# Kernel tuning notes

Hardware: AMD Instinct MI355X
Metric: run time of the kernel (lower is better)

## Reference

```python
import jax, jax.numpy as jnp
import numpy as np

BEAM = 64  # min(beam_size=64, num_states=512)


def setup_inputs() -> dict:
    key = jax.random.key(0)
    ks = jax.random.split(key, 8)
    B, N, S, E, F, D = 8, 1024, 512, 2048, 256, 32
    unaries = jax.random.normal(ks[0], (B, N, S), jnp.float32)
    masks = jnp.ones((B, N), dtype=bool)
    binary_edges = jax.random.randint(ks[1], (B, E, 2), 0, N)
    binary_masks = jnp.ones((B, E), dtype=bool)
    node_features = jax.random.normal(ks[2], (B, N, F), jnp.float32)
    targets = jax.random.randint(ks[3], (B, N), 0, S)
    # learned params
    bin_embed = jax.random.uniform(ks[4], (2, S, D), jnp.float32)  # torch.rand init
    W_dyn = jax.random.normal(ks[5], (2 * F, D * D), jnp.float32) / jnp.sqrt(2.0 * F)
    b_dyn = jnp.zeros((D * D,), jnp.float32)
    return dict(unaries=unaries, masks=masks, binary_edges=binary_edges,
                binary_masks=binary_masks, node_features=node_features,
                targets=targets, bin_embed=bin_embed, W_dyn=W_dyn, b_dyn=b_dyn)


def reference(unaries, masks, binary_edges, binary_masks, node_features,
              targets, bin_embed, W_dyn, b_dyn):
    B, N, S = unaries.shape
    D = bin_embed.shape[-1]
    mf = masks.astype(unaries.dtype)
    un = unaries * mf[..., None]  # mask unaries

    # put target state first in the beam (scatter +inf, then topk indices)
    big = jnp.asarray(1e30, un.dtype)
    _un = jax.lax.stop_gradient(un).at[
        jnp.arange(B)[:, None], jnp.arange(N)[None, :], targets].set(big)
    _, beam_targets = jax.lax.top_k(_un, BEAM)               # [B,N,K] int
    beam_unary = jnp.take_along_axis(un, beam_targets, axis=2)  # [B,N,K]

    # gather beam state-ids and node features at edge endpoints
    e0, e1 = binary_edges[..., 0], binary_edges[..., 1]      # [B,E]
    bt0 = jnp.take_along_axis(beam_targets, e0[:, :, None], axis=1)  # [B,E,K]
    bt1 = jnp.take_along_axis(beam_targets, e1[:, :, None], axis=1)
    s0 = bin_embed[0][bt0]                                   # [B,E,K,D]
    s1 = bin_embed[1][bt1]                                   # [B,E,K,D]
    f0 = jnp.take_along_axis(node_features, e0[:, :, None], axis=1)  # [B,E,F]
    f1 = jnp.take_along_axis(node_features, e1[:, :, None], axis=1)
    feat = jnp.concatenate([f0, f1], axis=-1)                # [B,E,2F]
    ew = jax.nn.relu(feat @ W_dyn + b_dyn)                   # [B,E,D*D]
    ew = ew.reshape(B, -1, D, D)                             # [B,E,D,D]

    # low-rank binary potentials: B E K1 D1, B E D1 D2, B E K2 D2 -> B E K1 K2
    bin_phis = jnp.einsum('beki,beij,belj->bekl', s0, ew, s1)

    # piecewise pseudo-likelihood
    norm_unary = jax.nn.log_softmax(beam_unary, axis=-1)
    gold_unary = jnp.where(masks, norm_unary[:, :, 0], 0.0)
    pll = gold_unary.sum(-1)                                 # [B]

    E = bin_phis.shape[1]
    norm_bin = jax.nn.log_softmax(bin_phis.reshape(B, E, BEAM * BEAM), axis=-1)
    gold_bin = jnp.where(binary_masks, norm_bin[:, :, 0], 0.0)  # index (0,0)
    pll = pll + gold_bin.sum(-1)

    nll = -(pll / mf.sum(-1)).mean()
    return nll
```

## Files before the change

### kernel.cpp

```cpp
#include <hip/hip_runtime.h>
#include <hip/hip_bf16.h>
#include <math.h>

#define BATCH  8
#define NNODE  1024
#define NSTATE 512
#define NEDGE  2048
#define NFEAT  256
#define DDIM   32
#define KBEAM  64

typedef __attribute__((ext_vector_type(8))) short bf16x8;
typedef __attribute__((ext_vector_type(4))) float f32x4;
typedef unsigned short u16;
typedef unsigned long long u64;

__device__ __forceinline__ u16 f2b(float f) {
  __hip_bfloat16 h = __float2bfloat16(f);
  return *reinterpret_cast<u16*>(&h);
}

__global__ __launch_bounds__(256) void beam_kernel(
    const float* __restrict__ unaries,
    const int*   __restrict__ targets,
    int*         __restrict__ beam_ids,
    float*       __restrict__ ugold)
{
  const int tid  = threadIdx.x;
  const int lane = tid & 63, wid = tid >> 6;
  const int node = blockIdx.x * 4 + wid;
  const float* row = unaries + (size_t)node * NSTATE;
  const int target = targets[node];

  float v[8];
  float4 va = *(const float4*)(row + lane * 4);
  float4 vb = *(const float4*)(row + 256 + lane * 4);
  v[0]=va.x; v[1]=va.y; v[2]=va.z; v[3]=va.w;
  v[4]=vb.x; v[5]=vb.y; v[6]=vb.z; v[7]=vb.w;

  u64 key[8]; int idx[8];
  #pragma unroll
  for (int t = 0; t < 8; t++) {
    int i = (t < 4) ? lane * 4 + t : 256 + lane * 4 + (t - 4);
    idx[t] = i;
    unsigned u = __float_as_uint(v[t]);
    unsigned k = (u & 0x80000000u) ? ~u : (u | 0x80000000u);
    if (i == target) k = 0xFFFFFFFFu;
    key[t] = ((u64)k << 9) | (unsigned)(NSTATE - 1 - i);
  }

  unsigned act = 0xFFu;
  int K = KBEAM;
  for (int b = 40; b >= 0; b--) {
    unsigned m1 = 0;
    #pragma unroll
    for (int t = 0; t < 8; t++)
      m1 |= ((unsigned)((key[t] >> b) & 1ull)) << t;
    unsigned ma = m1 & act;
    int c = 0;
    #pragma unroll
    for (int t = 0; t < 8; t++)
      c += __popcll(__ballot((ma >> t) & 1u));
    if (c >= K) act = ma; else { K -= c; act &= ~m1; }
  }
  u64 lm = __ballot(act != 0);
  int srclane = __ffsll((long long)lm) - 1;
  u64 thr = 0;
  #pragma unroll
  for (int t = 0; t < 8; t++) if ((act >> t) & 1u) thr = key[t];
  thr = __shfl(thr, srclane);

  unsigned sel = 0;
  #pragma unroll
  for (int t = 0; t < 8; t++) if (key[t] >= thr) sel |= 1u << t;

  float m = v[0];
  #pragma unroll
  for (int t = 1; t < 8; t++) m = fmaxf(m, v[t]);
  #pragma unroll
  for (int off = 32; off > 0; off >>= 1) m = fmaxf(m, __shfl_xor(m, off));
  float s = 0.0f;
  #pragma unroll
  for (int t = 0; t < 8; t++)
    if (sel & (1u << t)) s += __expf(v[t] - m);
  #pragma unroll
  for (int off = 32; off > 0; off >>= 1) s += __shfl_xor(s, off);

  int tl, ts;
  if (target < 256) { tl = target >> 2; ts = target & 3; }
  else { tl = (target - 256) >> 2; ts = 4 + ((target - 256) & 3); }
  float tvl = 0.0f;
  #pragma unroll
  for (int t = 0; t < 8; t++) if (t == ts) tvl = v[t];
  float tv = __shfl(tvl, tl);
  if (lane == 0) ugold[node] = tv - (m + __logf(s));

  int* bout = beam_ids + (size_t)node * KBEAM;
  unsigned selnt = sel;
  #pragma unroll
  for (int t = 0; t < 8; t++)
    if (idx[t] == target) { selnt &= ~(1u << t); bout[0] = target; }
  int base = 1;
  #pragma unroll
  for (int t = 0; t < 8; t++) {
    u64 bt = __ballot((selnt >> t) & 1u);
    if ((selnt >> t) & 1u) {
      int pos = base + __popcll(bt & ((1ull << lane) - 1ull));
      bout[pos] = idx[t];
    }
    base += __popcll(bt);
  }
}

__global__ __launch_bounds__(256) void conv_kernel(
    const float* __restrict__ W, u16* __restrict__ Wt,
    const float* __restrict__ bin_embed, u16* __restrict__ emb) {
  __shared__ u16 tile[64][64];
  const int tid = threadIdx.x;
  if (blockIdx.x >= 128) {
    int idx = ((blockIdx.x - 128) * 256 + tid) * 4;
    float4 v = *(const float4*)(bin_embed + idx);
    ushort4 o; o.x = f2b(v.x); o.y = f2b(v.y); o.z = f2b(v.z); o.w = f2b(v.w);
    *(ushort4*)(emb + idx) = o;
    return;
  }
  const int n0 = (blockIdx.x & 15) * 64;
  const int k0 = (blockIdx.x >> 4) * 64;
  #pragma unroll
  for (int p = 0; p < 4; p++) {
    int k  = (tid >> 4) + p * 16;
    int nc = (tid & 15) * 4;
    float4 v = *(const float4*)(W + (size_t)(k0 + k) * 1024 + n0 + nc);
    tile[nc + 0][k] = f2b(v.x); tile[nc + 1][k] = f2b(v.y);
    tile[nc + 2][k] = f2b(v.z); tile[nc + 3][k] = f2b(v.w);
  }
  __syncthreads();
  int n = tid >> 2, kc = (tid & 3) * 16;
  uint4 o0 = *(uint4*)&tile[n][kc];
  uint4 o1 = *(uint4*)&tile[n][kc + 8];
  *(uint4*)(Wt + (size_t)(n0 + n) * 512 + k0 + kc)     = o0;
  *(uint4*)(Wt + (size_t)(n0 + n) * 512 + k0 + kc + 8) = o1;
}

__global__ __launch_bounds__(128) void gatherA_kernel(
    const float* __restrict__ nf, const int* __restrict__ edges,
    u16* __restrict__ A) {
  const int eg = blockIdx.x;
  const int t  = threadIdx.x;
  const int b  = eg >> 11;
  const int n0 = edges[eg * 2 + 0], n1 = edges[eg * 2 + 1];
  const float* src = (t < 64)
      ? nf + ((size_t)(b * NNODE + n0) * NFEAT) + t * 4
      : nf + ((size_t)(b * NNODE + n1) * NFEAT) + (t - 64) * 4;
  float4 v = *(const float4*)src;
  ushort4 o; o.x = f2b(v.x); o.y = f2b(v.y); o.z = f2b(v.z); o.w = f2b(v.w);
  *(ushort4*)(A + (size_t)eg * 512 + t * 4) = o;
}

__global__ __launch_bounds__(256) void gemm_mfma_kernel(
    const u16* __restrict__ A,
    const u16* __restrict__ Bt,
    const float* __restrict__ bias,
    u16* __restrict__ ew)
{
  __shared__ u16 As[128 * 32];
  __shared__ u16 Bs[128 * 32];
  const int tid  = threadIdx.x;
  const int lane = tid & 63, wid = tid >> 6;
  const int wr = wid >> 1, wc = wid & 1;
  const int fr = lane & 15, fg = lane >> 4;
  const int row0 = blockIdx.y * 128, col0 = blockIdx.x * 128;

  const int r0 = wid * 32;
  const int rs = r0 + (lane >> 2);
  const int cs = (lane & 3) * 8;
  const u16* ga0 = A  + (size_t)(row0 + rs) * 512 + cs;
  const u16* ga1 = ga0 + (size_t)16 * 512;
  const u16* gb0 = Bt + (size_t)(col0 + rs) * 512 + cs;
  const u16* gb1 = gb0 + (size_t)16 * 512;
  u16* la0 = &As[r0 * 32];
  u16* la1 = &As[(r0 + 16) * 32];
  u16* lb0 = &Bs[r0 * 32];
  u16* lb1 = &Bs[(r0 + 16) * 32];

  f32x4 acc[4][4] = {};
  for (int ks = 0; ks < 16; ks++) {
    const int ko = ks * 32;
    __syncthreads();
    __builtin_amdgcn_global_load_lds(
        (const __attribute__((address_space(1))) unsigned int*)(ga0 + ko),
        (__attribute__((address_space(3))) unsigned int*)la0, 16, 0, 0);
    __builtin_amdgcn_global_load_lds(
        (const __attribute__((address_space(1))) unsigned int*)(ga1 + ko),
        (__attribute__((address_space(3))) unsigned int*)la1, 16, 0, 0);
    __builtin_amdgcn_global_load_lds(
        (const __attribute__((address_space(1))) unsigned int*)(gb0 + ko),
        (__attribute__((address_space(3))) unsigned int*)lb0, 16, 0, 0);
    __builtin_amdgcn_global_load_lds(
        (const __attribute__((address_space(1))) unsigned int*)(gb1 + ko),
        (__attribute__((address_space(3))) unsigned int*)lb1, 16, 0, 0);
    __syncthreads();

    bf16x8 af[4], bfr[4];
    #pragma unroll
    for (int mb = 0; mb < 4; mb++)
      af[mb] = *(bf16x8*)&As[(wr * 64 + mb * 16 + fr) * 32 + fg * 8];
    #pragma unroll
    for (int nb = 0; nb < 4; nb++)
      bfr[nb] = *(bf16x8*)&Bs[(wc * 64 + nb * 16 + fr) * 32 + fg * 8];
    #pragma unroll
    for (int mb = 0; mb < 4; mb++)
      #pragma unroll
      for (int nb = 0; nb < 4; nb++)
        acc[mb][nb] = __builtin_amdgcn_mfma_f32_16x16x32_bf16(
            af[mb], bfr[nb], acc[mb][nb], 0, 0, 0);
  }

  #pragma unroll
  for (int nb = 0; nb < 4; nb++) {
    int col = col0 + wc * 64 + nb * 16 + fr;
    float bc = bias[col];
    #pragma unroll
    for (int mb = 0; mb < 4; mb++) {
      #pragma unroll
      for (int r = 0; r < 4; r++) {
        int rowm = row0 + wr * 64 + mb * 16 + fg * 4 + r;
        float v = fmaxf(acc[mb][nb][r] + bc, 0.0f);
        ew[(size_t)rowm * 1024 + col] = f2b(v);
      }
    }
  }
}

__global__ __launch_bounds__(256) void edge_mfma_kernel(
    const u16* __restrict__ embed,
    const int* __restrict__ edges,
    const u16* __restrict__ ewb,
    const int* __restrict__ beam_ids,
    float*     __restrict__ egold)
{
  __shared__ u16 ush[4 * 2048];
  const int tid  = threadIdx.x;
  const int lane = tid & 63, wid = tid >> 6;
  u16* ul = &ush[wid * 2048];

  const int eg = blockIdx.x * 4 + wid;
  const int b  = eg >> 11;
  const int n0 = edges[eg * 2 + 0], n1 = edges[eg * 2 + 1];
  const int bt0 = beam_ids[(size_t)(b * NNODE + n0) * KBEAM + lane];
  const int bt1 = beam_ids[(size_t)(b * NNODE + n1) * KBEAM + lane];
  const int fr = lane & 15, fg = lane >> 4;

  bf16x8 a1[4], bew[2];
  #pragma unroll
  for (int mb = 0; mb < 4; mb++) {
    int r = __shfl(bt1, mb * 16 + fr);
    a1[mb] = *(const bf16x8*)(embed + (size_t)NSTATE * DDIM + (size_t)r * DDIM + fg * 8);
  }
  #pragma unroll
  for (int nb = 0; nb < 2; nb++)
    bew[nb] = *(const bf16x8*)(ewb + (size_t)eg * 1024 + (nb * 16 + fr) * 32 + fg * 8);
  f32x4 uacc[4][2] = {};
  #pragma unroll
  for (int mb = 0; mb < 4; mb++)
    #pragma unroll
    for (int nb = 0; nb < 2; nb++)
      uacc[mb][nb] = __builtin_amdgcn_mfma_f32_16x16x32_bf16(
          a1[mb], bew[nb], uacc[mb][nb], 0, 0, 0);

  #pragma unroll
  for (int mb = 0; mb < 4; mb++)
    #pragma unroll
    for (int nb = 0; nb < 2; nb++)
      #pragma unroll
      for (int r = 0; r < 4; r++)
        ul[(mb * 16 + fg * 4 + r) * 32 + nb * 16 + fr] = f2b(uacc[mb][nb][r]);
  asm volatile("s_waitcnt lgkmcnt(0)" ::: "memory");
  __builtin_amdgcn_sched_barrier(0);

  bf16x8 a0[4], bu[4];
  #pragma unroll
  for (int mb = 0; mb < 4; mb++) {
    int r = __shfl(bt0, mb * 16 + fr);
    a0[mb] = *(const bf16x8*)(embed + (size_t)r * DDIM + fg * 8);
  }
  #pragma unroll
  for (int nb = 0; nb < 4; nb++)
    bu[nb] = *(bf16x8*)&ul[(nb * 16 + fr) * 32 + fg * 8];
  f32x4 facc[4][4] = {};
  #pragma unroll
  for (int mb = 0; mb < 4; mb++)
    #pragma unroll
    for (int nb = 0; nb < 4; nb++)
      facc[mb][nb] = __builtin_amdgcn_mfma_f32_16x16x32_bf16(
          a0[mb], bu[nb], facc[mb][nb], 0, 0, 0);

  float mx = -INFINITY;
  #pragma unroll
  for (int mb = 0; mb < 4; mb++)
    #pragma unroll
    for (int nb = 0; nb < 4; nb++)
      #pragma unroll
      for (int r = 0; r < 4; r++) mx = fmaxf(mx, facc[mb][nb][r]);
  #pragma unroll
  for (int off = 32; off > 0; off >>= 1) mx = fmaxf(mx, __shfl_xor(mx, off));
  float s = 0.0f;
  #pragma unroll
  for (int mb = 0; mb < 4; mb++)
    #pragma unroll
    for (int nb = 0; nb < 4; nb++)
      #pragma unroll
      for (int r = 0; r < 4; r++) s += __expf(facc[mb][nb][r] - mx);
  #pragma unroll
  for (int off = 32; off > 0; off >>= 1) s += __shfl_xor(s, off);
  if (lane == 0) {
    egold[eg] = facc[0][0][0] - mx - __logf(s);
  }
}

__global__ __launch_bounds__(1024) void reduce_kernel(
    const float* __restrict__ ugold,
    const float* __restrict__ egold,
    float* __restrict__ out) {
  __shared__ float red[16];
  const int tid = threadIdx.x;
  float s = 0.0f;
  #pragma unroll
  for (int t = 0; t < 8; t++)  s += ugold[tid + t * 1024];
  #pragma unroll
  for (int t = 0; t < 16; t++) s += egold[tid + t * 1024];
  #pragma unroll
  for (int off = 32; off > 0; off >>= 1) s += __shfl_xor(s, off);
  if ((tid & 63) == 0) red[tid >> 6] = s;
  __syncthreads();
  if (tid == 0) {
    float tot = 0.0f;
    #pragma unroll
    for (int w = 0; w < 16; w++) tot += red[w];
    out[0] = -tot / (float)(BATCH * NNODE);
  }
}

extern "C" void kernel_launch(void* const* d_in, const int* in_sizes, int n_in,
                              void* d_out, int out_size, void* d_ws, size_t ws_size,
                              hipStream_t stream) {
  (void)in_sizes; (void)n_in; (void)out_size; (void)ws_size;
  const float* unaries   = (const float*)d_in[0];
  const int*   edges     = (const int*)  d_in[2];
  const float* nf        = (const float*)d_in[4];
  const int*   targets   = (const int*)  d_in[5];
  const float* bin_embed = (const float*)d_in[6];
  const float* W         = (const float*)d_in[7];
  const float* bias      = (const float*)d_in[8];
  float* out = (float*)d_out;

  char* ws = (char*)d_ws;
  float* ugold = (float*)ws;
  float* egold = (float*)(ws + (32u<<10));
  int*  beam_ids = (int*)(ws + (1u<<20));
  u16*  Abf = (u16*)(ws + (3u<<20));
  u16*  Wt  = (u16*)(ws + (19u<<20));
  u16*  ewb = (u16*)(ws + (20u<<20));
  u16*  emb = (u16*)(ws + (52u<<20));

  beam_kernel<<<BATCH * NNODE / 4, 256, 0, stream>>>(unaries, targets, beam_ids, ugold);
  conv_kernel<<<160, 256, 0, stream>>>(W, Wt, bin_embed, emb);
  gatherA_kernel<<<BATCH * NEDGE, 128, 0, stream>>>(nf, edges, Abf);
  gemm_mfma_kernel<<<dim3(8, 128), 256, 0, stream>>>(Abf, Wt, bias, ewb);
  edge_mfma_kernel<<<BATCH * NEDGE / 4, 256, 0, stream>>>(emb, edges, ewb, beam_ids, egold);
  reduce_kernel<<<1, 1024, 0, stream>>>(ugold, egold, out);
}
```

Baseline: 182.9 us.

## Merge prep kernels into one launch and fold final reduction into edge kernel

Merges the beam top-k, weight and embedding conversion, and feature gather kernels into a single prep kernel that dispatches on block index. The separate reduction kernel is removed: the edge kernel now uses an atomic counter so the last block to finish sums ugold and egold. The aim is to cut the launch count from six to three and shorten the serial tail. In exchange it adds an atomic, thread fences and a serial single-block reduction that runs at the end of the edge kernel.

New measurement: 441.0 us. 141% more time.

```diff
diff --git a/kernel.cpp b/kernel.cpp
--- a/kernel.cpp
+++ b/kernel.cpp
@@ -20,141 +20,140 @@
   return *reinterpret_cast<u16*>(&h);
 }
 
-__global__ __launch_bounds__(256) void beam_kernel(
-    const float* __restrict__ unaries,
-    const int*   __restrict__ targets,
-    int*         __restrict__ beam_ids,
-    float*       __restrict__ ugold)
+__global__ __launch_bounds__(256) void prep_kernel(
+    const float* __restrict__ unaries, const int* __restrict__ targets,
+    int* __restrict__ beam_ids, float* __restrict__ ugold,
+    const float* __restrict__ W, u16* __restrict__ Wt,
+    const float* __restrict__ bin_embed, u16* __restrict__ emb,
+    const float* __restrict__ nf, const int* __restrict__ edges,
+    u16* __restrict__ A, unsigned* __restrict__ counter)
 {
-  const int tid  = threadIdx.x;
+  __shared__ u16 tile[64][64];
+  const int blk = blockIdx.x;
+  const int tid = threadIdx.x;
   const int lane = tid & 63, wid = tid >> 6;
-  const int node = blockIdx.x * 4 + wid;
-  const float* row = unaries + (size_t)node * NSTATE;
-  const int target = targets[node];
-
-  float v[8];
-  float4 va = *(const float4*)(row + lane * 4);
-  float4 vb = *(const float4*)(row + 256 + lane * 4);
-  v[0]=va.x; v[1]=va.y; v[2]=va.z; v[3]=va.w;
-  v[4]=vb.x; v[5]=vb.y; v[6]=vb.z; v[7]=vb.w;
-
-  u64 key[8]; int idx[8];
-  #pragma unroll
-  for (int t = 0; t < 8; t++) {
-    int i = (t < 4) ? lane * 4 + t : 256 + lane * 4 + (t - 4);
-    idx[t] = i;
-    unsigned u = __float_as_uint(v[t]);
-    unsigned k = (u & 0x80000000u) ? ~u : (u | 0x80000000u);
-    if (i == target) k = 0xFFFFFFFFu;
-    key[t] = ((u64)k << 9) | (unsigned)(NSTATE - 1 - i);
-  }
-
-  unsigned act = 0xFFu;
-  int K = KBEAM;
-  for (int b = 40; b >= 0; b--) {
-    unsigned m1 = 0;
+  if (blk == 0 && tid == 0) *counter = 0u;
+
+  if (blk < 2048) {
+    const int node = blk * 4 + wid;
+    const float* row = unaries + (size_t)node * NSTATE;
+    const int target = targets[node];
+
+    float v[8];
+    float4 va = *(const float4*)(row + lane * 4);
+    float4 vb = *(const float4*)(row + 256 + lane * 4);
+    v[0]=va.x; v[1]=va.y; v[2]=va.z; v[3]=va.w;
+    v[4]=vb.x; v[5]=vb.y; v[6]=vb.z; v[7]=vb.w;
+
+    u64 key[8]; int idx[8];
+    #pragma unroll
+    for (int t = 0; t < 8; t++) {
+      int i = (t < 4) ? lane * 4 + t : 256 + lane * 4 + (t - 4);
+      idx[t] = i;
+      unsigned u = __float_as_uint(v[t]);
+      unsigned k = (u & 0x80000000u) ? ~u : (u | 0x80000000u);
+      if (i == target) k = 0xFFFFFFFFu;
+      key[t] = ((u64)k << 9) | (unsigned)(NSTATE - 1 - i);
+    }
+
+    unsigned act = 0xFFu;
+    int K = KBEAM;
+    for (int b = 40; b >= 0; b--) {
+      unsigned m1 = 0;
+      #pragma unroll
+      for (int t = 0; t < 8; t++)
+        m1 |= ((unsigned)((key[t] >> b) & 1ull)) << t;
+      unsigned ma = m1 & act;
+      int c = 0;
+      #pragma unroll
+      for (int t = 0; t < 8; t++)
+        c += __popcll(__ballot((ma >> t) & 1u));
+      if (c >= K) act = ma; else { K -= c; act &= ~m1; }
+    }
+    u64 lm = __ballot(act != 0);
+    int srclane = __ffsll((long long)lm) - 1;
+    u64 thr = 0;
+    #pragma unroll
+    for (int t = 0; t < 8; t++) if ((act >> t) & 1u) thr = key[t];
+    thr = __shfl(thr, srclane);
+
+    unsigned sel = 0;
+    #pragma unroll
+    for (int t = 0; t < 8; t++) if (key[t] >= thr) sel |= 1u << t;
+
+    float m = v[0];
+    #pragma unroll
+    for (int t = 1; t < 8; t++) m = fmaxf(m, v[t]);
+    #pragma unroll
+    for (int off = 32; off > 0; off >>= 1) m = fmaxf(m, __shfl_xor(m, off));
+    float s = 0.0f;
     #pragma unroll
     for (int t = 0; t < 8; t++)
-      m1 |= ((unsigned)((key[t] >> b) & 1ull)) << t;
-    unsigned ma = m1 & act;
-    int c = 0;
+      if (sel & (1u << t)) s += __expf(v[t] - m);
+    #pragma unroll
+    for (int off = 32; off > 0; off >>= 1) s += __shfl_xor(s, off);
+
+    int tl, ts;
+    if (target < 256) { tl = target >> 2; ts = target & 3; }
+    else { tl = (target - 256) >> 2; ts = 4 + ((target - 256) & 3); }
+    float tvl = 0.0f;
+    #pragma unroll
+    for (int t = 0; t < 8; t++) if (t == ts) tvl = v[t];
+    float tv = __shfl(tvl, tl);
+    if (lane == 0) ugold[node] = tv - (m + __logf(s));
+
+    int* bout = beam_ids + (size_t)node * KBEAM;
+    unsigned selnt = sel;
     #pragma unroll
     for (int t = 0; t < 8; t++)
-      c += __popcll(__ballot((ma >> t) & 1u));
-    if (c >= K) act = ma; else { K -= c; act &= ~m1; }
-  }
-  u64 lm = __ballot(act != 0);
-  int srclane = __ffsll((long long)lm) - 1;
-  u64 thr = 0;
-  #pragma unroll
-  for (int t = 0; t < 8; t++) if ((act >> t) & 1u) thr = key[t];
-  thr = __shfl(thr, srclane);
-
-  unsigned sel = 0;
-  #pragma unroll
-  for (int t = 0; t < 8; t++) if (key[t] >= thr) sel |= 1u << t;
-
-  float m = v[0];
-  #pragma unroll
-  for (int t = 1; t < 8; t++) m = fmaxf(m, v[t]);
-  #pragma unroll
-  for (int off = 32; off > 0; off >>= 1) m = fmaxf(m, __shfl_xor(m, off));
-  float s = 0.0f;
-  #pragma unroll
-  for (int t = 0; t < 8; t++)
-    if (sel & (1u << t)) s += __expf(v[t] - m);
-  #pragma unroll
-  for (int off = 32; off > 0; off >>= 1) s += __shfl_xor(s, off);
-
-  int tl, ts;
-  if (target < 256) { tl = target >> 2; ts = target & 3; }
-  else { tl = (target - 256) >> 2; ts = 4 + ((target - 256) & 3); }
-  float tvl = 0.0f;
-  #pragma unroll
-  for (int t = 0; t < 8; t++) if (t == ts) tvl = v[t];
-  float tv = __shfl(tvl, tl);
-  if (lane == 0) ugold[node] = tv - (m + __logf(s));
-
-  int* bout = beam_ids + (size_t)node * KBEAM;
-  unsigned selnt = sel;
-  #pragma unroll
-  for (int t = 0; t < 8; t++)
-    if (idx[t] == target) { selnt &= ~(1u << t); bout[0] = target; }
-  int base = 1;
-  #pragma unroll
-  for (int t = 0; t < 8; t++) {
-    u64 bt = __ballot((selnt >> t) & 1u);
-    if ((selnt >> t) & 1u) {
-      int pos = base + __popcll(bt & ((1ull << lane) - 1ull));
-      bout[pos] = idx[t];
-    }
-    base += __popcll(bt);
-  }
-}
-
-__global__ __launch_bounds__(256) void conv_kernel(
-    const float* __restrict__ W, u16* __restrict__ Wt,
-    const float* __restrict__ bin_embed, u16* __restrict__ emb) {
-  __shared__ u16 tile[64][64];
-  const int tid = threadIdx.x;
-  if (blockIdx.x >= 128) {
-    int idx = ((blockIdx.x - 128) * 256 + tid) * 4;
+      if (idx[t] == target) { selnt &= ~(1u << t); bout[0] = target; }
+    int base = 1;
+    #pragma unroll
+    for (int t = 0; t < 8; t++) {
+      u64 bt = __ballot((selnt >> t) & 1u);
+      if ((selnt >> t) & 1u) {
+        int pos = base + __popcll(bt & ((1ull << lane) - 1ull));
+        bout[pos] = idx[t];
+      }
+      base += __popcll(bt);
+    }
+  } else if (blk < 2176) {
+    const int bb = blk - 2048;
+    const int n0 = (bb & 15) * 64;
+    const int k0 = (bb >> 4) * 64;
+    #pragma unroll
+    for (int p = 0; p < 4; p++) {
+      int k  = (tid >> 4) + p * 16;
+      int nc = (tid & 15) * 4;
+      float4 v = *(const float4*)(W + (size_t)(k0 + k) * 1024 + n0 + nc);
+      tile[nc + 0][k] = f2b(v.x); tile[nc + 1][k] = f2b(v.y);
+      tile[nc + 2][k] = f2b(v.z); tile[nc + 3][k] = f2b(v.w);
+    }
+    __syncthreads();
+    int n = tid >> 2, kc = (tid & 3) * 16;
+    uint4 o0 = *(uint4*)&tile[n][kc];
+    uint4 o1 = *(uint4*)&tile[n][kc + 8];
+    *(uint4*)(Wt + (size_t)(n0 + n) * 512 + k0 + kc)     = o0;
+    *(uint4*)(Wt + (size_t)(n0 + n) * 512 + k0 + kc + 8) = o1;
+  } else if (blk < 2208) {
+    int idx = ((blk - 2176) * 256 + tid) * 4;
     float4 v = *(const float4*)(bin_embed + idx);
     ushort4 o; o.x = f2b(v.x); o.y = f2b(v.y); o.z = f2b(v.z); o.w = f2b(v.w);
     *(ushort4*)(emb + idx) = o;
-    return;
-  }
-  const int n0 = (blockIdx.x & 15) * 64;
-  const int k0 = (blockIdx.x >> 4) * 64;
-  #pragma unroll
-  for (int p = 0; p < 4; p++) {
-    int k  = (tid >> 4) + p * 16;
-    int nc = (tid & 15) * 4;
-    float4 v = *(const float4*)(W + (size_t)(k0 + k) * 1024 + n0 + nc);
-    tile[nc + 0][k] = f2b(v.x); tile[nc + 1][k] = f2b(v.y);
-    tile[nc + 2][k] = f2b(v.z); tile[nc + 3][k] = f2b(v.w);
-  }
-  __syncthreads();
-  int n = tid >> 2, kc = (tid & 3) * 16;
-  uint4 o0 = *(uint4*)&tile[n][kc];
-  uint4 o1 = *(uint4*)&tile[n][kc + 8];
-  *(uint4*)(Wt + (size_t)(n0 + n) * 512 + k0 + kc)     = o0;
-  *(uint4*)(Wt + (size_t)(n0 + n) * 512 + k0 + kc + 8) = o1;
-}
-
-__global__ __launch_bounds__(128) void gatherA_kernel(
-    const float* __restrict__ nf, const int* __restrict__ edges,
-    u16* __restrict__ A) {
-  const int eg = blockIdx.x;
-  const int t  = threadIdx.x;
-  const int b  = eg >> 11;
-  const int n0 = edges[eg * 2 + 0], n1 = edges[eg * 2 + 1];
-  const float* src = (t < 64)
-      ? nf + ((size_t)(b * NNODE + n0) * NFEAT) + t * 4
-      : nf + ((size_t)(b * NNODE + n1) * NFEAT) + (t - 64) * 4;
-  float4 v = *(const float4*)src;
-  ushort4 o; o.x = f2b(v.x); o.y = f2b(v.y); o.z = f2b(v.z); o.w = f2b(v.w);
-  *(ushort4*)(A + (size_t)eg * 512 + t * 4) = o;
+  } else {
+    const int eg = (blk - 2208) * 4 + wid;
+    const int b  = eg >> 11;
+    const int n0 = edges[eg * 2 + 0], n1 = edges[eg * 2 + 1];
+    const int nd = (lane < 32) ? n0 : n1;
+    const int off = (lane & 31) * 8;
+    const float* src = nf + ((size_t)(b * NNODE + nd) * NFEAT) + off;
+    float4 v0 = *(const float4*)src;
+    float4 v1 = *(const float4*)(src + 4);
+    u16 o[8];
+    o[0]=f2b(v0.x); o[1]=f2b(v0.y); o[2]=f2b(v0.z); o[3]=f2b(v0.w);
+    o[4]=f2b(v1.x); o[5]=f2b(v1.y); o[6]=f2b(v1.z); o[7]=f2b(v1.w);
+    *(uint4*)(A + (size_t)eg * 512 + lane * 8) = *(uint4*)o;
+  }
 }
 
 __global__ __launch_bounds__(256) void gemm_mfma_kernel(
@@ -237,9 +236,14 @@
     const int* __restrict__ edges,
     const u16* __restrict__ ewb,
     const int* __restrict__ beam_ids,
-    float*     __restrict__ egold)
+    float*     __restrict__ egold,
+    const float* __restrict__ ugold,
+    unsigned*  __restrict__ counter,
+    float*     __restrict__ out)
 {
   __shared__ u16 ush[4 * 2048];
+  __shared__ float red[4];
+  __shared__ unsigned lastf;
   const int tid  = threadIdx.x;
   const int lane = tid & 63, wid = tid >> 6;
   u16* ul = &ush[wid * 2048];
@@ -316,28 +320,23 @@
   if (lane == 0) {
     egold[eg] = facc[0][0][0] - mx - __logf(s);
   }
-}
-
-__global__ __launch_bounds__(1024) void reduce_kernel(
-    const float* __restrict__ ugold,
-    const float* __restrict__ egold,
-    float* __restrict__ out) {
-  __shared__ float red[16];
-  const int tid = threadIdx.x;
-  float s = 0.0f;
-  #pragma unroll
-  for (int t = 0; t < 8; t++)  s += ugold[tid + t * 1024];
-  #pragma unroll
-  for (int t = 0; t < 16; t++) s += egold[tid + t * 1024];
-  #pragma unroll
-  for (int off = 32; off > 0; off >>= 1) s += __shfl_xor(s, off);
-  if ((tid & 63) == 0) red[tid >> 6] = s;
+
+  __threadfence();
   __syncthreads();
-  if (tid == 0) {
-    float tot = 0.0f;
-    #pragma unroll
-    for (int w = 0; w < 16; w++) tot += red[w];
-    out[0] = -tot / (float)(BATCH * NNODE);
+  if (tid == 0)
+    lastf = (atomicAdd(counter, 1u) == (unsigned)(gridDim.x - 1)) ? 1u : 0u;
+  __syncthreads();
+  if (lastf) {
+    __threadfence();
+    float t = 0.0f;
+    for (int i = tid; i < BATCH * NNODE; i += 256) t += ugold[i];
+    for (int i = tid; i < BATCH * NEDGE; i += 256) t += egold[i];
+    #pragma unroll
+    for (int off = 32; off > 0; off >>= 1) t += __shfl_xor(t, off);
+    if ((tid & 63) == 0) red[tid >> 6] = t;
+    __syncthreads();
+    if (tid == 0)
+      out[0] = -(red[0] + red[1] + red[2] + red[3]) / (float)(BATCH * NNODE);
   }
 }
 
@@ -357,16 +356,17 @@
   char* ws = (char*)d_ws;
   float* ugold = (float*)ws;
   float* egold = (float*)(ws + (32u<<10));
+  unsigned* counter = (unsigned*)(ws + (96u<<10));
   int*  beam_ids = (int*)(ws + (1u<<20));
   u16*  Abf = (u16*)(ws + (3u<<20));
   u16*  Wt  = (u16*)(ws + (19u<<20));
   u16*  ewb = (u16*)(ws + (20u<<20));
   u16*  emb = (u16*)(ws + (52u<<20));
 
-  beam_kernel<<<BATCH * NNODE / 4, 256, 0, stream>>>(unaries, targets, beam_ids, ugold);
-  conv_kernel<<<160, 256, 0, stream>>>(W, Wt, bin_embed, emb);
-  gatherA_kernel<<<BATCH * NEDGE, 128, 0, stream>>>(nf, edges, Abf);
+  prep_kernel<<<6304, 256, 0, stream>>>(unaries, targets, beam_ids, ugold,
+                                        W, Wt, bin_embed, emb,
+                                        nf, edges, Abf, counter);
   gemm_mfma_kernel<<<dim3(8, 128), 256, 0, stream>>>(Abf, Wt, bias, ewb);
-  edge_mfma_kernel<<<BATCH * NEDGE / 4, 256, 0, stream>>>(emb, edges, ewb, beam_ids, egold);
-  reduce_kernel<<<1, 1024, 0, stream>>>(ugold, egold, out);
-}
+  edge_mfma_kernel<<<BATCH * NEDGE / 4, 256, 0, stream>>>(
+      emb, edges, ewb, beam_ids, egold, ugold, counter, out);
+}
```
